# Kernel tuning notes

Hardware: AMD Instinct MI355X
Metric: run time of the kernel (lower is better)

## Reference

```python
import jax, jax.numpy as jnp
import numpy as np

N0, N1, N2 = 331776, 36864, 4096   # src nodes block0, mid nodes, final items
E0, E1, EP = 294912, 32768, 4096   # edges block0, block1, pos/neg edges
F_RAW, D, H = 128, 256, 512        # raw feat dim, hidden_dims_sum, 2*hidden
N_NODES = 1000000                  # global graph node count (scorer bias)


def setup_inputs() -> dict:
    key = jax.random.key(0)
    ks = jax.random.split(key, 24)
    ri = lambda k, n, hi: jax.random.randint(k, (n,), 0, hi, dtype=jnp.int64 if False else jnp.int32).astype(jnp.int32)
    s = 0.05
    return {
        "feat0": jax.random.normal(ks[0], (N0, F_RAW), jnp.float32),
        "feat_dst": jax.random.normal(ks[1], (N2, F_RAW), jnp.float32),
        "weights0": jax.random.uniform(ks[2], (E0,), jnp.float32),
        "weights1": jax.random.uniform(ks[3], (E1,), jnp.float32),
        "W_proj": jax.random.normal(ks[4], (F_RAW, D), jnp.float32) * s,
        "b_proj": jnp.zeros((D,), jnp.float32),
        "Q1": jax.random.normal(ks[5], (D, H), jnp.float32) * s,
        "bq1": jnp.zeros((H,), jnp.float32),
        "W1": jax.random.normal(ks[6], (D + H, D), jnp.float32) * s,
        "bw1": jnp.zeros((D,), jnp.float32),
        "Q2": jax.random.normal(ks[7], (D, H), jnp.float32) * s,
        "bq2": jnp.zeros((H,), jnp.float32),
        "W2": jax.random.normal(ks[8], (D + H, D), jnp.float32) * s,
        "bw2": jnp.zeros((D,), jnp.float32),
        "bias": jnp.zeros((N_NODES,), jnp.float32),
        "block0_src": ri(ks[9], E0, N0),
        "block0_dst": ri(ks[10], E0, N1),
        "block1_src": ri(ks[11], E1, N1),
        "block1_dst": ri(ks[12], E1, N2),
        "pos_src": ri(ks[13], EP, N2),
        "pos_dst": ri(ks[14], EP, N2),
        "neg_src": ri(ks[15], EP, N2),
        "neg_dst": ri(ks[16], EP, N2),
        "nid": ri(ks[17], N2, N_NODES),
    }


def _l2norm(z):
    n = jnp.linalg.norm(z, axis=1, keepdims=True)
    return z / jnp.where(n == 0, 1.0, n)


def _sage_conv(h_src, h_dst, src, dst, w, Q, bq, W, bw, n_dst):
    # WeightedSAGEConv (dropout omitted: eval-mode deterministic reference)
    n = jax.nn.relu(h_src @ Q + bq)                                   # [N_src, H]
    m = jax.ops.segment_sum(n[src] * w[:, None], dst, num_segments=n_dst)
    ws = jnp.clip(jax.ops.segment_sum(w, dst, num_segments=n_dst), 1.0, None)
    z = jax.nn.relu(jnp.concatenate([m / ws[:, None], h_dst], axis=1) @ W + bw)
    return _l2norm(z)


def _score(h, src, dst, nid, bias):
    # ItemToItemScorer: u_dot_v + src/dst node bias
    return jnp.sum(h[src] * h[dst], axis=1) + bias[nid[src]] + bias[nid[dst]]


def reference(feat0, feat_dst, weights0, weights1, W_proj, b_proj, Q1, bq1, W1, bw1,
              Q2, bq2, W2, bw2, bias, block0_src, block0_dst, block1_src, block1_dst,
              pos_src, pos_dst, neg_src, neg_dst, nid):
    h = feat0 @ W_proj + b_proj                                         # LinearProjector
    h = _sage_conv(h, h[:N1], block0_src, block0_dst, weights0, Q1, bq1, W1, bw1, N1)
    h = _sage_conv(h, h[:N2], block1_src, block1_dst, weights1, Q2, bq2, W2, bw2, N2)
    h_item = (feat_dst @ W_proj + b_proj) + h                           # get_repr skip-add
    pos_score = _score(h_item, pos_src, pos_dst, nid, bias)
    neg_score = _score(h_item, neg_src, neg_dst, nid, bias)
    return (pos_score, neg_score)
```

## Files before the change

### kernel.cpp

```cpp
#include <hip/hip_runtime.h>
#include <hip/hip_bf16.h>

typedef __hip_bfloat16 bf16;
typedef __attribute__((ext_vector_type(8))) short frag8;
typedef __attribute__((ext_vector_type(4))) float f32x4;

#define N0c 331776
#define N1c 36864
#define N2c 4096
#define E0c 294912
#define E1c 32768

__device__ __forceinline__ float bfbits2f(unsigned short b) {
    union { unsigned u; float f; } x; x.u = ((unsigned)b) << 16; return x.f;
}
__device__ __forceinline__ unsigned short f2bfbits(float f) {
    bf16 h = __float2bfloat16(f);
    return *reinterpret_cast<unsigned short*>(&h);
}
__device__ __forceinline__ void load4f(const float* p, float* o) {
    const float4 v = *reinterpret_cast<const float4*>(p);
    o[0] = v.x; o[1] = v.y; o[2] = v.z; o[3] = v.w;
}
__device__ __forceinline__ ushort4 pack4(float4 v) {
    ushort4 o; o.x = f2bfbits(v.x); o.y = f2bfbits(v.y);
    o.z = f2bfbits(v.z); o.w = f2bfbits(v.w); return o;
}
__device__ __forceinline__ void store_c(float* p, float v) { *p = v; }
__device__ __forceinline__ void store_c(bf16* p, float v)  { *p = __float2bfloat16(v); }
__device__ __forceinline__ f32x4 zero4() {
    f32x4 z; z[0] = 0.f; z[1] = 0.f; z[2] = 0.f; z[3] = 0.f; return z;
}
__device__ __forceinline__ f32x4 mfma16(frag8 a, frag8 b, f32x4 c) {
    return __builtin_amdgcn_mfma_f32_16x16x32_bf16(a, b, c, 0, 0, 0);
}

__global__ __launch_bounds__(256) void transpose_bf16(
    const float* __restrict__ src, bf16* __restrict__ dst, int K, int N)
{
    const int idx = blockIdx.x * 256 + threadIdx.x;
    if (idx >= K * N) return;
    const int k = idx / N, n = idx - k * N;
    dst[(size_t)n * K + k] = __float2bfloat16(src[idx]);
}

__global__ __launch_bounds__(256) void hist_kernel(
    const int* __restrict__ dst, int* __restrict__ cnt, int E)
{
    const int e = blockIdx.x * 256 + threadIdx.x;
    if (e < E) atomicAdd(&cnt[dst[e]], 1);
}

__global__ __launch_bounds__(256) void scan_kernel(
    const int* __restrict__ cnt, int* __restrict__ base, int n)
{
    __shared__ int ps[256];
    const int t = threadIdx.x;
    const int chunk = (n + 255) >> 8;
    const int lo = t * chunk;
    const int hi = (lo + chunk < n) ? lo + chunk : n;
    int s = 0;
    for (int i = lo; i < hi; ++i) s += cnt[i];
    ps[t] = s;
    __syncthreads();
    for (int off = 1; off < 256; off <<= 1) {
        int v = (t >= off) ? ps[t - off] : 0;
        __syncthreads();
        ps[t] += v;
        __syncthreads();
    }
    int run = ps[t] - s;
    for (int i = lo; i < hi; ++i) { base[i] = run; run += cnt[i]; }
    if (t == 255) base[n] = ps[255];
}

__global__ __launch_bounds__(256) void fill_kernel(
    const int* __restrict__ dst, const int* __restrict__ base,
    int* __restrict__ cursor, int* __restrict__ perm, int E)
{
    const int e = blockIdx.x * 256 + threadIdx.x;
    if (e < E) {
        const int d = dst[e];
        const int p = base[d] + atomicAdd(&cursor[d], 1);
        perm[p] = e;
    }
}

template<typename TC>
__global__ __launch_bounds__(256) void gemm_mfma_proj(
    const float* __restrict__ A, const bf16* __restrict__ WpT,
    const float* __restrict__ bp, TC* __restrict__ C)
{
    __shared__ bf16 Xs[64 * 136];

    const int tid = threadIdx.x;
    const int lane = tid & 63, wave = tid >> 6;
    const int row0 = blockIdx.x * 64;

    {
        const int r = tid >> 2, q = tid & 3;
        const float* ar = A + (size_t)(row0 + r) * 128 + q * 32;
        bf16* xr = Xs + r * 136 + q * 32;
        #pragma unroll
        for (int i = 0; i < 8; ++i)
            *reinterpret_cast<ushort4*>(xr + i * 4) =
                pack4(*reinterpret_cast<const float4*>(ar + i * 4));
    }
    __syncthreads();

    const int lr = lane & 15;
    const int lk = (lane >> 4) * 8;
    const int lm4 = (lane >> 4) * 4;

    f32x4 acc[4][4];
    #pragma unroll
    for (int mi = 0; mi < 4; ++mi)
        #pragma unroll
        for (int ni = 0; ni < 4; ++ni) acc[mi][ni] = zero4();

    #pragma unroll
    for (int kk = 0; kk < 4; ++kk) {
        frag8 a[4], b[4];
        #pragma unroll
        for (int mi = 0; mi < 4; ++mi)
            a[mi] = *reinterpret_cast<const frag8*>(&Xs[(mi * 16 + lr) * 136 + kk * 32 + lk]);
        #pragma unroll
        for (int ni = 0; ni < 4; ++ni)
            b[ni] = *reinterpret_cast<const frag8*>(
                WpT + (size_t)(wave * 64 + ni * 16 + lr) * 128 + kk * 32 + lk);
        #pragma unroll
        for (int mi = 0; mi < 4; ++mi)
            #pragma unroll
            for (int ni = 0; ni < 4; ++ni)
                acc[mi][ni] = mfma16(a[mi], b[ni], acc[mi][ni]);
    }

    #pragma unroll
    for (int ni = 0; ni < 4; ++ni) {
        const int c = wave * 64 + ni * 16 + lr;
        const float bb = bp[c];
        #pragma unroll
        for (int mi = 0; mi < 4; ++mi)
            #pragma unroll
            for (int i = 0; i < 4; ++i)
                store_c(C + (size_t)(row0 + mi * 16 + lm4 + i) * 256 + c,
                        acc[mi][ni][i] + bb);
    }
}

__global__ __launch_bounds__(256) void edge_csr(
    const bf16* __restrict__ zn, const bf16* __restrict__ QT,
    const float* __restrict__ bq,
    const int* __restrict__ perm, const int* __restrict__ src,
    const float* __restrict__ w,
    bf16* __restrict__ nbuf)
{
    __shared__ bf16 Zs[64 * 264];
    __shared__ int   srcs[64];
    __shared__ float wts[64];

    const int tid = threadIdx.x;
    const int lane = tid & 63, wave = tid >> 6;
    const size_t p0 = (size_t)blockIdx.x * 64;

    if (tid < 64) {
        const int e = perm[p0 + tid];
        srcs[tid] = src[e];
        wts[tid]  = w[e];
    }
    __syncthreads();

    {
        const int r = tid >> 2, q = tid & 3;
        const bf16* zr = zn + (size_t)srcs[r] * 256 + q * 64;
        bf16* zo = Zs + r * 264 + q * 64;
        #pragma unroll
        for (int i = 0; i < 16; ++i)
            *reinterpret_cast<ushort4*>(zo + i * 4) =
                *reinterpret_cast<const ushort4*>(zr + i * 4);
    }
    __syncthreads();

    const int lr = lane & 15;
    const int lk = (lane >> 4) * 8;
    const int lm4 = (lane >> 4) * 4;

    #pragma unroll
    for (int pass = 0; pass < 2; ++pass) {
        const int nc0 = wave * 128 + pass * 64;
        f32x4 acc[4][4];
        #pragma unroll
        for (int mi = 0; mi < 4; ++mi)
            #pragma unroll
            for (int ni = 0; ni < 4; ++ni) acc[mi][ni] = zero4();

        #pragma unroll
        for (int kk = 0; kk < 8; ++kk) {
            frag8 a[4], b[4];
            #pragma unroll
            for (int mi = 0; mi < 4; ++mi)
                a[mi] = *reinterpret_cast<const frag8*>(&Zs[(mi * 16 + lr) * 264 + kk * 32 + lk]);
            #pragma unroll
            for (int ni = 0; ni < 4; ++ni)
                b[ni] = *reinterpret_cast<const frag8*>(
                    QT + (size_t)(nc0 + ni * 16 + lr) * 256 + kk * 32 + lk);
            #pragma unroll
            for (int mi = 0; mi < 4; ++mi)
                #pragma unroll
                for (int ni = 0; ni < 4; ++ni)
                    acc[mi][ni] = mfma16(a[mi], b[ni], acc[mi][ni]);
        }
        #pragma unroll
        for (int ni = 0; ni < 4; ++ni) {
            const int c = nc0 + ni * 16 + lr;
            const float bb = bq[c];
            #pragma unroll
            for (int mi = 0; mi < 4; ++mi)
                #pragma unroll
                for (int i = 0; i < 4; ++i) {
                    const int row = mi * 16 + lm4 + i;
                    const float val = fmaxf(acc[mi][ni][i] + bb, 0.f) * wts[row];
                    nbuf[(p0 + row) * 512 + c] = __float2bfloat16(val);
                }
        }
    }
}

__global__ __launch_bounds__(256) void reduce_csr(
    const bf16* __restrict__ nbuf, const int* __restrict__ base,
    const int* __restrict__ perm, const float* __restrict__ w,
    bf16* __restrict__ mout)
{
    const int d = blockIdx.x;
    const int lo = base[d], hi = base[d + 1];
    __shared__ float s_inv;
    if (threadIdx.x == 0) {
        float s = 0.f;
        for (int k = lo; k < hi; ++k) s += w[perm[k]];
        s_inv = 1.f / fmaxf(s, 1.f);
    }
    __syncthreads();
    const int c = threadIdx.x * 2;
    float a0 = 0.f, a1 = 0.f;
    for (int k = lo; k < hi; ++k) {
        const ushort2 u = *reinterpret_cast<const ushort2*>(nbuf + (size_t)k * 512 + c);
        a0 += bfbits2f(u.x); a1 += bfbits2f(u.y);
    }
    ushort2 o; o.x = f2bfbits(a0 * s_inv); o.y = f2bfbits(a1 * s_inv);
    *reinterpret_cast<ushort2*>(mout + (size_t)d * 512 + c) = o;
}

template<typename TC>
__global__ __launch_bounds__(256) void gemm_mfma_concat(
    const bf16* __restrict__ m, const bf16* __restrict__ hdst,
    const bf16* __restrict__ WT, const float* __restrict__ bias,
    TC* __restrict__ C)
{
    __shared__ bf16 As[64 * 136];

    const int tid = threadIdx.x;
    const int lane = tid & 63, wave = tid >> 6;
    const int row0 = blockIdx.x * 64;
    const int r = tid >> 2, q = tid & 3;

    const int lr = lane & 15;
    const int lk = (lane >> 4) * 8;
    const int lm4 = (lane >> 4) * 4;

    f32x4 acc[4][4];
    #pragma unroll
    for (int mi = 0; mi < 4; ++mi)
        #pragma unroll
        for (int ni = 0; ni < 4; ++ni) acc[mi][ni] = zero4();

    #pragma unroll
    for (int ch = 0; ch < 6; ++ch) {
        bf16* xr = As + r * 136 + q * 32;
        const bf16* srcp = (ch < 4)
            ? m    + (size_t)(row0 + r) * 512 + ch * 128 + q * 32
            : hdst + (size_t)(row0 + r) * 256 + (ch - 4) * 128 + q * 32;
        #pragma unroll
        for (int i = 0; i < 8; ++i)
            *reinterpret_cast<ushort4*>(xr + i * 4) =
                *reinterpret_cast<const ushort4*>(srcp + i * 4);
        __syncthreads();

        #pragma unroll
        for (int kk = 0; kk < 4; ++kk) {
            frag8 a[4], b[4];
            #pragma unroll
            for (int mi = 0; mi < 4; ++mi)
                a[mi] = *reinterpret_cast<const frag8*>(&As[(mi * 16 + lr) * 136 + kk * 32 + lk]);
            #pragma unroll
            for (int ni = 0; ni < 4; ++ni)
                b[ni] = *reinterpret_cast<const frag8*>(
                    WT + (size_t)(wave * 64 + ni * 16 + lr) * 768 + ch * 128 + kk * 32 + lk);
            #pragma unroll
            for (int mi = 0; mi < 4; ++mi)
                #pragma unroll
                for (int ni = 0; ni < 4; ++ni)
                    acc[mi][ni] = mfma16(a[mi], b[ni], acc[mi][ni]);
        }
        __syncthreads();
    }

    #pragma unroll
    for (int ni = 0; ni < 4; ++ni) {
        const int c = wave * 64 + ni * 16 + lr;
        const float bb = bias[c];
        #pragma unroll
        for (int mi = 0; mi < 4; ++mi)
            #pragma unroll
            for (int i = 0; i < 4; ++i)
                store_c(C + (size_t)(row0 + mi * 16 + lm4 + i) * 256 + c,
                        fmaxf(acc[mi][ni][i] + bb, 0.f));
    }
}

__global__ __launch_bounds__(256) void l2norm_kernel(
    const bf16* __restrict__ Z, bf16* __restrict__ out, int rows)
{
    const int wave = threadIdx.x >> 6, lane = threadIdx.x & 63;
    const int row = blockIdx.x * 4 + wave;
    if (row >= rows) return;
    const ushort4 u = *reinterpret_cast<const ushort4*>(Z + (size_t)row * 256 + lane * 4);
    float v[4] = { bfbits2f(u.x), bfbits2f(u.y), bfbits2f(u.z), bfbits2f(u.w) };
    float ss = v[0]*v[0] + v[1]*v[1] + v[2]*v[2] + v[3]*v[3];
    #pragma unroll
    for (int off = 32; off; off >>= 1) ss += __shfl_xor(ss, off, 64);
    const float scale = (ss == 0.f) ? 1.f : (1.f / sqrtf(ss));
    ushort4 o;
    o.x = f2bfbits(v[0]*scale); o.y = f2bfbits(v[1]*scale);
    o.z = f2bfbits(v[2]*scale); o.w = f2bfbits(v[3]*scale);
    *reinterpret_cast<ushort4*>(out + (size_t)row * 256 + lane * 4) = o;
}

__global__ __launch_bounds__(256) void l2norm_add_kernel(
    const float* __restrict__ Z, const float* __restrict__ P,
    float* __restrict__ out, int rows)
{
    const int wave = threadIdx.x >> 6, lane = threadIdx.x & 63;
    const int row = blockIdx.x * 4 + wave;
    if (row >= rows) return;
    float v[4];
    load4f(Z + (size_t)row * 256 + lane * 4, v);
    float ss = v[0]*v[0] + v[1]*v[1] + v[2]*v[2] + v[3]*v[3];
    #pragma unroll
    for (int off = 32; off; off >>= 1) ss += __shfl_xor(ss, off, 64);
    const float scale = (ss == 0.f) ? 1.f : (1.f / sqrtf(ss));
    float p[4];
    load4f(P + (size_t)row * 256 + lane * 4, p);
    float4 o;
    o.x = p[0] + v[0]*scale; o.y = p[1] + v[1]*scale;
    o.z = p[2] + v[2]*scale; o.w = p[3] + v[3]*scale;
    *reinterpret_cast<float4*>(out + (size_t)row * 256 + lane * 4) = o;
}

__global__ __launch_bounds__(256) void score_kernel(
    const float* __restrict__ h,
    const int* __restrict__ ps, const int* __restrict__ pdi,
    const int* __restrict__ ns, const int* __restrict__ nd,
    const int* __restrict__ nid, const float* __restrict__ bias,
    float* __restrict__ out)
{
    const int wave = threadIdx.x >> 6, lane = threadIdx.x & 63;
    const int e = blockIdx.x * 4 + wave;
    const int ei = e & 4095;
    const int s = (e < 4096) ? ps[ei] : ns[ei];
    const int d = (e < 4096) ? pdi[ei] : nd[ei];
    float a[4], b[4];
    load4f(h + (size_t)s * 256 + lane * 4, a);
    load4f(h + (size_t)d * 256 + lane * 4, b);
    float dot = a[0]*b[0] + a[1]*b[1] + a[2]*b[2] + a[3]*b[3];
    #pragma unroll
    for (int off = 32; off; off >>= 1) dot += __shfl_xor(dot, off, 64);
    if (lane == 0)
        out[e] = dot + bias[nid[s]] + bias[nid[d]];
}

extern "C" void kernel_launch(void* const* d_in, const int* in_sizes, int n_in,
                              void* d_out, int out_size, void* d_ws, size_t ws_size,
                              hipStream_t stream)
{
    const float* feat0    = (const float*)d_in[0];
    const float* feat_dst = (const float*)d_in[1];
    const float* weights0 = (const float*)d_in[2];
    const float* weights1 = (const float*)d_in[3];
    const float* W_proj   = (const float*)d_in[4];
    const float* b_proj   = (const float*)d_in[5];
    const float* Q1       = (const float*)d_in[6];
    const float* bq1      = (const float*)d_in[7];
    const float* W1       = (const float*)d_in[8];
    const float* bw1      = (const float*)d_in[9];
    const float* Q2       = (const float*)d_in[10];
    const float* bq2      = (const float*)d_in[11];
    const float* W2       = (const float*)d_in[12];
    const float* bw2      = (const float*)d_in[13];
    const float* biasN    = (const float*)d_in[14];
    const int* b0s = (const int*)d_in[15];
    const int* b0d = (const int*)d_in[16];
    const int* b1s = (const int*)d_in[17];
    const int* b1d = (const int*)d_in[18];
    const int* pos_src = (const int*)d_in[19];
    const int* pos_dst = (const int*)d_in[20];
    const int* neg_src = (const int*)d_in[21];
    const int* neg_dst = (const int*)d_in[22];
    const int* nid     = (const int*)d_in[23];

    char* ws = (char*)d_ws;
    size_t off = 0;
    auto alloc = [&](size_t bytes) -> void* {
        void* p = ws + off; off += (bytes + 255) & ~(size_t)255; return p;
    };
    bf16* h0    = (bf16*)alloc((size_t)N0c * 256 * 2);
    char* r2    = (char*)alloc((size_t)E0c * 512 * 2);
    bf16* m1    = (bf16*)alloc((size_t)N1c * 512 * 2);
    bf16* WpT   = (bf16*)alloc((size_t)256 * 128 * 2);
    bf16* Q1T   = (bf16*)alloc((size_t)512 * 256 * 2);
    bf16* Q2T   = (bf16*)alloc((size_t)512 * 256 * 2);
    bf16* W1T   = (bf16*)alloc((size_t)256 * 768 * 2);
    bf16* W2T   = (bf16*)alloc((size_t)256 * 768 * 2);
    int*  cnt    = (int*)alloc((size_t)(N1c + 1) * 4);
    int*  base   = (int*)alloc((size_t)(N1c + 1) * 4);
    int*  cursor = (int*)alloc((size_t)N1c * 4);
    int*  perm   = (int*)alloc((size_t)E0c * 4);

    bf16* nbuf1 = (bf16*)r2;
    bf16* z1b   = (bf16*)r2;
    bf16* z1n   = (bf16*)(r2 + 18874368);
    bf16* nbuf2 = (bf16*)(r2 + 37748736);
    bf16* m2    = (bf16*)(r2 + 71303168);
    float* z2     = (float*)(r2 + 75497472);
    float* pdbuf  = (float*)(r2 + 79691776);
    float* h_item = (float*)(r2 + 83886080);

    transpose_bf16<<<(128*256 + 255)/256, 256, 0, stream>>>(W_proj, WpT, 128, 256);
    transpose_bf16<<<(256*512 + 255)/256, 256, 0, stream>>>(Q1, Q1T, 256, 512);
    transpose_bf16<<<(256*512 + 255)/256, 256, 0, stream>>>(Q2, Q2T, 256, 512);
    transpose_bf16<<<(768*256 + 255)/256, 256, 0, stream>>>(W1, W1T, 768, 256);
    transpose_bf16<<<(768*256 + 255)/256, 256, 0, stream>>>(W2, W2T, 768, 256);

    gemm_mfma_proj<bf16><<<N0c/64, 256, 0, stream>>>(feat0, WpT, b_proj, h0);

    hipMemsetAsync(cnt,    0, (size_t)N1c * 4, stream);
    hipMemsetAsync(cursor, 0, (size_t)N1c * 4, stream);
    hist_kernel<<<E0c/256, 256, 0, stream>>>(b0d, cnt, E0c);
    scan_kernel<<<1, 256, 0, stream>>>(cnt, base, N1c);
    fill_kernel<<<E0c/256, 256, 0, stream>>>(b0d, base, cursor, perm, E0c);

    edge_csr<<<E0c/64, 256, 0, stream>>>(h0, Q1T, bq1, perm, b0s, weights0, nbuf1);

    reduce_csr<<<N1c, 256, 0, stream>>>(nbuf1, base, perm, weights0, m1);

    gemm_mfma_concat<bf16><<<N1c/64, 256, 0, stream>>>(m1, h0, W1T, bw1, z1b);

    l2norm_kernel<<<N1c/4, 256, 0, stream>>>(z1b, z1n, N1c);

    hipMemsetAsync(cnt,    0, (size_t)N2c * 4, stream);
    hipMemsetAsync(cursor, 0, (size_t)N2c * 4, stream);
    hist_kernel<<<E1c/256, 256, 0, stream>>>(b1d, cnt, E1c);
    scan_kernel<<<1, 256, 0, stream>>>(cnt, base, N2c);
    fill_kernel<<<E1c/256, 256, 0, stream>>>(b1d, base, cursor, perm, E1c);

    edge_csr<<<E1c/64, 256, 0, stream>>>(z1n, Q2T, bq2, perm, b1s, weights1, nbuf2);

    reduce_csr<<<N2c, 256, 0, stream>>>(nbuf2, base, perm, weights1, m2);

    gemm_mfma_concat<float><<<N2c/64, 256, 0, stream>>>(m2, z1n, W2T, bw2, z2);

    gemm_mfma_proj<float><<<N2c/64, 256, 0, stream>>>(feat_dst, WpT, b_proj, pdbuf);

    l2norm_add_kernel<<<N2c/4, 256, 0, stream>>>(z2, pdbuf, h_item, N2c);

    score_kernel<<<2048, 256, 0, stream>>>(
        h_item, pos_src, pos_dst, neg_src, neg_dst, nid, biasN, (float*)d_out);
}
```

Baseline: 793.0 us.

## Fuse edge message GEMM with segmented reduction via fp32 atomics

The per-edge message kernel now reduces its 64 sorted edges in shared memory by destination run and atomically adds the normalised partial sums into an fp32 aggregate. This removes the large bf16 per-edge message buffer and the separate per-destination reduce kernel. Weight sums are computed with atomics in the histogram pass and inverted once. The scan now uses 1024 threads with int4 loads. The trade-offs are atomic contention, a memset of the fp32 aggregate, nondeterministic summation order, and fp32 reads in the concat GEMM.

```diff
diff --git a/kernel.cpp b/kernel.cpp
--- a/kernel.cpp
+++ b/kernel.cpp
@@ -14,6 +14,9 @@
 __device__ __forceinline__ float bfbits2f(unsigned short b) {
     union { unsigned u; float f; } x; x.u = ((unsigned)b) << 16; return x.f;
 }
+__device__ __forceinline__ float bfval2f(const bf16* p) {
+    return bfbits2f(*reinterpret_cast<const unsigned short*>(p));
+}
 __device__ __forceinline__ unsigned short f2bfbits(float f) {
     bf16 h = __float2bfloat16(f);
     return *reinterpret_cast<unsigned short*>(&h);
@@ -45,25 +48,40 @@
 }
 
 __global__ __launch_bounds__(256) void hist_kernel(
-    const int* __restrict__ dst, int* __restrict__ cnt, int E)
+    const int* __restrict__ dst, const float* __restrict__ w,
+    int* __restrict__ cnt, float* __restrict__ wsum, int E)
 {
     const int e = blockIdx.x * 256 + threadIdx.x;
-    if (e < E) atomicAdd(&cnt[dst[e]], 1);
-}
-
-__global__ __launch_bounds__(256) void scan_kernel(
+    if (e < E) {
+        const int d = dst[e];
+        atomicAdd(&cnt[d], 1);
+        atomicAdd(&wsum[d], w[e]);
+    }
+}
+
+__global__ __launch_bounds__(256) void invws_kernel(
+    const float* __restrict__ wsum, float* __restrict__ invws, int n)
+{
+    const int i = blockIdx.x * 256 + threadIdx.x;
+    if (i < n) invws[i] = 1.f / fmaxf(wsum[i], 1.f);
+}
+
+__global__ __launch_bounds__(1024) void scan_kernel(
     const int* __restrict__ cnt, int* __restrict__ base, int n)
 {
-    __shared__ int ps[256];
+    __shared__ int ps[1024];
     const int t = threadIdx.x;
-    const int chunk = (n + 255) >> 8;
+    const int chunk = (n + 1023) >> 10;
     const int lo = t * chunk;
     const int hi = (lo + chunk < n) ? lo + chunk : n;
     int s = 0;
-    for (int i = lo; i < hi; ++i) s += cnt[i];
+    for (int i = lo; i < hi; i += 4) {
+        const int4 v = *reinterpret_cast<const int4*>(cnt + i);
+        s += v.x + v.y + v.z + v.w;
+    }
     ps[t] = s;
     __syncthreads();
-    for (int off = 1; off < 256; off <<= 1) {
+    for (int off = 1; off < 1024; off <<= 1) {
         int v = (t >= off) ? ps[t - off] : 0;
         __syncthreads();
         ps[t] += v;
@@ -71,7 +89,7 @@
     }
     int run = ps[t] - s;
     for (int i = lo; i < hi; ++i) { base[i] = run; run += cnt[i]; }
-    if (t == 255) base[n] = ps[255];
+    if (t == 1023) base[n] = ps[1023];
 }
 
 __global__ __launch_bounds__(256) void fill_kernel(
@@ -148,15 +166,17 @@
     }
 }
 
-__global__ __launch_bounds__(256) void edge_csr(
+__global__ __launch_bounds__(256) void edge_reduce_csr(
     const bf16* __restrict__ zn, const bf16* __restrict__ QT,
     const float* __restrict__ bq,
-    const int* __restrict__ perm, const int* __restrict__ src,
-    const float* __restrict__ w,
-    bf16* __restrict__ nbuf)
+    const int* __restrict__ perm, const int* __restrict__ srcv,
+    const int* __restrict__ dstv, const float* __restrict__ w,
+    const float* __restrict__ invws, float* __restrict__ mout)
 {
     __shared__ bf16 Zs[64 * 264];
+    __shared__ bf16 Os[64 * 264];
     __shared__ int   srcs[64];
+    __shared__ int   dsts[64];
     __shared__ float wts[64];
 
     const int tid = threadIdx.x;
@@ -165,7 +185,8 @@
 
     if (tid < 64) {
         const int e = perm[p0 + tid];
-        srcs[tid] = src[e];
+        srcs[tid] = srcv[e];
+        dsts[tid] = dstv[e];
         wts[tid]  = w[e];
     }
     __syncthreads();
@@ -185,7 +206,6 @@
     const int lk = (lane >> 4) * 8;
     const int lm4 = (lane >> 4) * 4;
 
-    #pragma unroll
     for (int pass = 0; pass < 2; ++pass) {
         const int nc0 = wave * 128 + pass * 64;
         f32x4 acc[4][4];
@@ -210,49 +230,45 @@
                 for (int ni = 0; ni < 4; ++ni)
                     acc[mi][ni] = mfma16(a[mi], b[ni], acc[mi][ni]);
         }
+
         #pragma unroll
         for (int ni = 0; ni < 4; ++ni) {
-            const int c = nc0 + ni * 16 + lr;
-            const float bb = bq[c];
+            const int gc = nc0 + ni * 16 + lr;
+            const float bb = bq[gc];
+            const int lc = wave * 64 + ni * 16 + lr;
             #pragma unroll
             for (int mi = 0; mi < 4; ++mi)
                 #pragma unroll
                 for (int i = 0; i < 4; ++i) {
                     const int row = mi * 16 + lm4 + i;
                     const float val = fmaxf(acc[mi][ni][i] + bb, 0.f) * wts[row];
-                    nbuf[(p0 + row) * 512 + c] = __float2bfloat16(val);
+                    Os[row * 264 + lc] = __float2bfloat16(val);
                 }
         }
-    }
-}
-
-__global__ __launch_bounds__(256) void reduce_csr(
-    const bf16* __restrict__ nbuf, const int* __restrict__ base,
-    const int* __restrict__ perm, const float* __restrict__ w,
-    bf16* __restrict__ mout)
-{
-    const int d = blockIdx.x;
-    const int lo = base[d], hi = base[d + 1];
-    __shared__ float s_inv;
-    if (threadIdx.x == 0) {
-        float s = 0.f;
-        for (int k = lo; k < hi; ++k) s += w[perm[k]];
-        s_inv = 1.f / fmaxf(s, 1.f);
-    }
-    __syncthreads();
-    const int c = threadIdx.x * 2;
-    float a0 = 0.f, a1 = 0.f;
-    for (int k = lo; k < hi; ++k) {
-        const ushort2 u = *reinterpret_cast<const ushort2*>(nbuf + (size_t)k * 512 + c);
-        a0 += bfbits2f(u.x); a1 += bfbits2f(u.y);
-    }
-    ushort2 o; o.x = f2bfbits(a0 * s_inv); o.y = f2bfbits(a1 * s_inv);
-    *reinterpret_cast<ushort2*>(mout + (size_t)d * 512 + c) = o;
+        __syncthreads();
+
+        {
+            const int L = tid;
+            const int gc = (L >> 6) * 128 + pass * 64 + (L & 63);
+            float a = 0.f;
+            int cur = dsts[0];
+            for (int r = 0; r < 64; ++r) {
+                const int d = dsts[r];
+                if (d != cur) {
+                    atomicAdd(&mout[(size_t)cur * 512 + gc], a * invws[cur]);
+                    a = 0.f; cur = d;
+                }
+                a += bfval2f(&Os[r * 264 + L]);
+            }
+            atomicAdd(&mout[(size_t)cur * 512 + gc], a * invws[cur]);
+        }
+        __syncthreads();
+    }
 }
 
 template<typename TC>
 __global__ __launch_bounds__(256) void gemm_mfma_concat(
-    const bf16* __restrict__ m, const bf16* __restrict__ hdst,
+    const float* __restrict__ m, const bf16* __restrict__ hdst,
     const bf16* __restrict__ WT, const float* __restrict__ bias,
     TC* __restrict__ C)
 {
@@ -276,13 +292,19 @@
     #pragma unroll
     for (int ch = 0; ch < 6; ++ch) {
         bf16* xr = As + r * 136 + q * 32;
-        const bf16* srcp = (ch < 4)
-            ? m    + (size_t)(row0 + r) * 512 + ch * 128 + q * 32
-            : hdst + (size_t)(row0 + r) * 256 + (ch - 4) * 128 + q * 32;
-        #pragma unroll
-        for (int i = 0; i < 8; ++i)
-            *reinterpret_cast<ushort4*>(xr + i * 4) =
-                *reinterpret_cast<const ushort4*>(srcp + i * 4);
+        if (ch < 4) {
+            const float* sp = m + (size_t)(row0 + r) * 512 + ch * 128 + q * 32;
+            #pragma unroll
+            for (int i = 0; i < 8; ++i)
+                *reinterpret_cast<ushort4*>(xr + i * 4) =
+                    pack4(*reinterpret_cast<const float4*>(sp + i * 4));
+        } else {
+            const bf16* sp = hdst + (size_t)(row0 + r) * 256 + (ch - 4) * 128 + q * 32;
+            #pragma unroll
+            for (int i = 0; i < 8; ++i)
+                *reinterpret_cast<ushort4*>(xr + i * 4) =
+                    *reinterpret_cast<const ushort4*>(sp + i * 4);
+        }
         __syncthreads();
 
         #pragma unroll
@@ -412,27 +434,25 @@
     auto alloc = [&](size_t bytes) -> void* {
         void* p = ws + off; off += (bytes + 255) & ~(size_t)255; return p;
     };
-    bf16* h0    = (bf16*)alloc((size_t)N0c * 256 * 2);
-    char* r2    = (char*)alloc((size_t)E0c * 512 * 2);
-    bf16* m1    = (bf16*)alloc((size_t)N1c * 512 * 2);
-    bf16* WpT   = (bf16*)alloc((size_t)256 * 128 * 2);
-    bf16* Q1T   = (bf16*)alloc((size_t)512 * 256 * 2);
-    bf16* Q2T   = (bf16*)alloc((size_t)512 * 256 * 2);
-    bf16* W1T   = (bf16*)alloc((size_t)256 * 768 * 2);
-    bf16* W2T   = (bf16*)alloc((size_t)256 * 768 * 2);
-    int*  cnt    = (int*)alloc((size_t)(N1c + 1) * 4);
-    int*  base   = (int*)alloc((size_t)(N1c + 1) * 4);
-    int*  cursor = (int*)alloc((size_t)N1c * 4);
-    int*  perm   = (int*)alloc((size_t)E0c * 4);
-
-    bf16* nbuf1 = (bf16*)r2;
-    bf16* z1b   = (bf16*)r2;
-    bf16* z1n   = (bf16*)(r2 + 18874368);
-    bf16* nbuf2 = (bf16*)(r2 + 37748736);
-    bf16* m2    = (bf16*)(r2 + 71303168);
-    float* z2     = (float*)(r2 + 75497472);
-    float* pdbuf  = (float*)(r2 + 79691776);
-    float* h_item = (float*)(r2 + 83886080);
+    bf16*  h0     = (bf16*) alloc((size_t)N0c * 256 * 2);
+    float* m1     = (float*)alloc((size_t)N1c * 512 * 4);
+    bf16*  z1b    = (bf16*) alloc((size_t)N1c * 256 * 2);
+    bf16*  z1n    = (bf16*) alloc((size_t)N1c * 256 * 2);
+    float* m2     = (float*)alloc((size_t)N2c * 512 * 4);
+    float* z2     = (float*)alloc((size_t)N2c * 256 * 4);
+    float* pdbuf  = (float*)alloc((size_t)N2c * 256 * 4);
+    float* h_item = (float*)alloc((size_t)N2c * 256 * 4);
+    bf16*  WpT    = (bf16*) alloc((size_t)256 * 128 * 2);
+    bf16*  Q1T    = (bf16*) alloc((size_t)512 * 256 * 2);
+    bf16*  Q2T    = (bf16*) alloc((size_t)512 * 256 * 2);
+    bf16*  W1T    = (bf16*) alloc((size_t)256 * 768 * 2);
+    bf16*  W2T    = (bf16*) alloc((size_t)256 * 768 * 2);
+    int*   cnt    = (int*)  alloc((size_t)(N1c + 1) * 4);
+    int*   base   = (int*)  alloc((size_t)(N1c + 1) * 4);
+    int*   cursor = (int*)  alloc((size_t)N1c * 4);
+    float* wsumf  = (float*)alloc((size_t)N1c * 4);
+    float* invws  = (float*)alloc((size_t)N1c * 4);
+    int*   perm   = (int*)  alloc((size_t)E0c * 4);
 
     transpose_bf16<<<(128*256 + 255)/256, 256, 0, stream>>>(W_proj, WpT, 128, 256);
     transpose_bf16<<<(256*512 + 255)/256, 256, 0, stream>>>(Q1, Q1T, 256, 512);
@@ -444,32 +464,33 @@
 
     hipMemsetAsync(cnt,    0, (size_t)N1c * 4, stream);
     hipMemsetAsync(cursor, 0, (size_t)N1c * 4, stream);
-    hist_kernel<<<E0c/256, 256, 0, stream>>>(b0d, cnt, E0c);
-    scan_kernel<<<1, 256, 0, stream>>>(cnt, base, N1c);
+    hipMemsetAsync(wsumf,  0, (size_t)N1c * 4, stream);
+    hist_kernel<<<E0c/256, 256, 0, stream>>>(b0d, weights0, cnt, wsumf, E0c);
+    scan_kernel<<<1, 1024, 0, stream>>>(cnt, base, N1c);
     fill_kernel<<<E0c/256, 256, 0, stream>>>(b0d, base, cursor, perm, E0c);
-
-    edge_csr<<<E0c/64, 256, 0, stream>>>(h0, Q1T, bq1, perm, b0s, weights0, nbuf1);
-
-    reduce_csr<<<N1c, 256, 0, stream>>>(nbuf1, base, perm, weights0, m1);
+    invws_kernel<<<(N1c + 255)/256, 256, 0, stream>>>(wsumf, invws, N1c);
+
+    hipMemsetAsync(m1, 0, (size_t)N1c * 512 * 4, stream);
+    edge_reduce_csr<<<E0c/64, 256, 0, stream>>>(
+        h0, Q1T, bq1, perm, b0s, b0d, weights0, invws, m1);
 
     gemm_mfma_concat<bf16><<<N1c/64, 256, 0, stream>>>(m1, h0, W1T, bw1, z1b);
-
     l2norm_kernel<<<N1c/4, 256, 0, stream>>>(z1b, z1n, N1c);
 
     hipMemsetAsync(cnt,    0, (size_t)N2c * 4, stream);
     hipMemsetAsync(cursor, 0, (size_t)N2c * 4, stream);
-    hist_kernel<<<E1c/256, 256, 0, stream>>>(b1d, cnt, E1c);
-    scan_kernel<<<1, 256, 0, stream>>>(cnt, base, N2c);
+    hipMemsetAsync(wsumf,  0, (size_t)N2c * 4, stream);
+    hist_kernel<<<E1c/256, 256, 0, stream>>>(b1d, weights1, cnt, wsumf, E1c);
+    scan_kernel<<<1, 1024, 0, stream>>>(cnt, base, N2c);
     fill_kernel<<<E1c/256, 256, 0, stream>>>(b1d, base, cursor, perm, E1c);
-
-    edge_csr<<<E1c/64, 256, 0, stream>>>(z1n, Q2T, bq2, perm, b1s, weights1, nbuf2);
-
-    reduce_csr<<<N2c, 256, 0, stream>>>(nbuf2, base, perm, weights1, m2);
+    invws_kernel<<<(N2c + 255)/256, 256, 0, stream>>>(wsumf, invws, N2c);
+
+    hipMemsetAsync(m2, 0, (size_t)N2c * 512 * 4, stream);
+    edge_reduce_csr<<<E1c/64, 256, 0, stream>>>(
+        z1n, Q2T, bq2, perm, b1s, b1d, weights1, invws, m2);
 
     gemm_mfma_concat<float><<<N2c/64, 256, 0, stream>>>(m2, z1n, W2T, bw2, z2);
-
     gemm_mfma_proj<float><<<N2c/64, 256, 0, stream>>>(feat_dst, WpT, b_proj, pdbuf);
-
     l2norm_add_kernel<<<N2c/4, 256, 0, stream>>>(z2, pdbuf, h_item, N2c);
 
     score_kernel<<<2048, 256, 0, stream>>>(
```

Measured after the change: 691.1 us. 1.15x faster.
